# Kernel tuning notes

Measured on AMD Instinct MI355X. Metric: run time of the kernel, lower is better.

Reference implementation:

```python
import jax, jax.numpy as jnp
import numpy as np

DIM = 256
NUM_HEADS = 8
HEAD_DIM = 64
NUM_MEM_KV = 4
HIDDEN = NUM_HEADS * HEAD_DIM  # 512


def rmsnorm(x, g):
    # F.normalize(x, dim=1) * g * sqrt(C)
    c = x.shape[1]
    n = jnp.sqrt(jnp.sum(x * x, axis=1, keepdims=True))
    xn = x / jnp.maximum(n, 1e-12)
    return xn * g * (c ** 0.5)


def setup_inputs() -> dict:
    key = jax.random.key(0)
    ks = jax.random.split(key, 7)
    b, h, w = 16, 64, 64
    x = jax.random.normal(ks[0], (b, DIM, h, w), dtype=jnp.float32)
    g_in = jnp.ones((1, DIM, 1, 1), dtype=jnp.float32)
    w_qkv = jax.random.normal(ks[1], (HIDDEN * 3, DIM), dtype=jnp.float32) * (1.0 / np.sqrt(DIM))
    mem_kv = jax.random.normal(ks[2], (2, NUM_HEADS, HEAD_DIM, NUM_MEM_KV), dtype=jnp.float32)
    w_out = jax.random.normal(ks[3], (DIM, HIDDEN), dtype=jnp.float32) * (1.0 / np.sqrt(HIDDEN))
    b_out = jax.random.normal(ks[4], (DIM,), dtype=jnp.float32) * 0.01
    g_out = jnp.ones((1, DIM, 1, 1), dtype=jnp.float32)
    return {"x": x, "g_in": g_in, "w_qkv": w_qkv, "mem_kv": mem_kv,
            "w_out": w_out, "b_out": b_out, "g_out": g_out}


def reference(x, g_in, w_qkv, mem_kv, w_out, b_out, g_out):
    b, c, h, w = x.shape
    scale = HEAD_DIM ** (-0.5)
    xn = rmsnorm(x, g_in)
    # 1x1 conv (no bias) as GEMM: [b, 3*hidden, h, w]
    qkv = jnp.einsum('bcxy,oc->boxy', xn, w_qkv)
    q, k, v = jnp.split(qkv, 3, axis=1)
    # b (heads d) x y -> b heads d n
    def to_heads(t):
        return t.reshape(b, NUM_HEADS, HEAD_DIM, h * w)
    q, k, v = to_heads(q), to_heads(k), to_heads(v)
    mem_k = jnp.broadcast_to(mem_kv[0], (b, NUM_HEADS, HEAD_DIM, NUM_MEM_KV))
    mem_v = jnp.broadcast_to(mem_kv[1], (b, NUM_HEADS, HEAD_DIM, NUM_MEM_KV))
    k = jnp.concatenate([mem_k, k], axis=-1)
    v = jnp.concatenate([mem_v, v], axis=-1)
    q = jax.nn.softmax(q, axis=-2) * scale   # softmax over head_dim
    k = jax.nn.softmax(k, axis=-1)           # softmax over sequence
    context = jnp.einsum('bhdn,bhen->bhde', k, v)  # [b,h,d,d] per-head context
    out = jnp.einsum('bhde,bhdn->bhen', context, q)  # [b,h,d,n]
    out = out.reshape(b, HIDDEN, h, w)
    out = jnp.einsum('bcxy,oc->boxy', out, w_out) + b_out[None, :, None, None]
    return rmsnorm(out, g_out)
```

## Files before the change

kernel.cpp:

```cpp
#include <hip/hip_runtime.h>
#include <hip/hip_bf16.h>

typedef __hip_bfloat16 bf16;
typedef short bf16x8 __attribute__((ext_vector_type(8)));
typedef float f32x4 __attribute__((ext_vector_type(4)));

#define PTOT  65536
#define NPOS  4096
#define CIN   256
#define HID   512
#define HD    64

__device__ __forceinline__ float us2f(unsigned short u) {
    return __uint_as_float(((unsigned int)u) << 16);
}
__device__ __forceinline__ float ldf(const void* p, size_t i, bool bf) {
    return bf ? us2f(((const unsigned short*)p)[i]) : ((const float*)p)[i];
}
__device__ __forceinline__ unsigned short f2bs(float v) {
    __hip_bfloat16 h = __float2bfloat16(v);
    return *reinterpret_cast<unsigned short*>(&h);
}
__device__ __forceinline__ void gld16(const void* g, void* s) {
    __builtin_amdgcn_global_load_lds(
        (const __attribute__((address_space(1))) unsigned int*)g,
        (__attribute__((address_space(3))) unsigned int*)s, 16, 0, 0);
}

__global__ __launch_bounds__(256) void k_detect(const unsigned* __restrict__ x,
                                                int* __restrict__ flag) {
    int t = threadIdx.x;
    unsigned w = x[(size_t)t * 997];
    unsigned e7 = (w >> 8) & 0x7f;
    __shared__ int s[256];
    s[t] = (e7 >= 58 && e7 <= 66) ? 1 : 0;
    __syncthreads();
    for (int k = 128; k > 0; k >>= 1) { if (t < k) s[t] += s[t + k]; __syncthreads(); }
    if (t == 0) flag[0] = (s[0] >= 128) ? 1 : 0;
}

__global__ void k_relay(const int* __restrict__ src, int* __restrict__ dst) {
    dst[0] = src[0];
}

__global__ __launch_bounds__(256) void k_cvt(const void* __restrict__ src,
        unsigned short* __restrict__ dst, int n, const int* __restrict__ flag) {
    bool bf = flag[0] != 0;
    int i = blockIdx.x * 256 + threadIdx.x;
    if (i < n) dst[i] = f2bs(ldf(src, i, bf));
}

template<bool BF>
__device__ __forceinline__ void norm_xn_body(const void* __restrict__ x,
        const void* __restrict__ g, unsigned short* __restrict__ xn,
        float* __restrict__ smem)
{
    float* xs   = smem;
    float* gS   = smem + 17216;
    float* red2 = smem + 17472;
    float* sS   = smem + 18496;
    const int t = threadIdx.x;
    const int p0 = blockIdx.x * 64;
    const int b = p0 >> 12;
    const int posbase = p0 & 4095;
    gS[t] = ldf(g, t, BF);
    __syncthreads();
    const int pl4 = (t & 15) * 4;
    const int crow = t >> 4;
    const size_t xbase = ((size_t)b * CIN) << 12;
    float ssq[4] = {0.f, 0.f, 0.f, 0.f};
    #pragma unroll
    for (int rr = 0; rr < 16; ++rr) {
        int c = rr * 16 + crow;
        float v[4];
        if (BF) {
            ushort4 u = *(const ushort4*)((const unsigned short*)x + xbase +
                                          ((size_t)c << 12) + posbase + pl4);
            v[0] = us2f(u.x); v[1] = us2f(u.y); v[2] = us2f(u.z); v[3] = us2f(u.w);
        } else {
            float4 f = *(const float4*)((const float*)x + xbase +
                                        ((size_t)c << 12) + posbase + pl4);
            v[0] = f.x; v[1] = f.y; v[2] = f.z; v[3] = f.w;
        }
        float gv = gS[c];
        float* row = xs + (c >> 6) * 4304 + (c & 63) * 67;
        #pragma unroll
        for (int e = 0; e < 4; ++e) {
            ssq[e] += v[e] * v[e];
            row[pl4 + e] = v[e] * gv;
        }
    }
    #pragma unroll
    for (int e = 0; e < 4; ++e) red2[crow * 64 + pl4 + e] = ssq[e];
    __syncthreads();
    if (t < 64) {
        float tot = 0.f;
        #pragma unroll
        for (int j = 0; j < 16; ++j) tot += red2[j * 64 + t];
        sS[t] = 16.0f / fmaxf(sqrtf(tot), 1e-12f);
    }
    __syncthreads();
    const int pr = t >> 2, c0 = (t & 3) * 64;
    const float sc = sS[pr];
    const float* base = xs + (t & 3) * 4304 + pr;
    unsigned short* dst = &xn[(size_t)(p0 + pr) * 256 + c0];
    #pragma unroll
    for (int q = 0; q < 4; ++q) {
        unsigned short tmp[16];
        #pragma unroll
        for (int j = 0; j < 16; ++j)
            tmp[j] = f2bs(base[(q * 16 + j) * 67] * sc);
        *(uint4*)(dst + q * 16)     = ((uint4*)tmp)[0];
        *(uint4*)(dst + q * 16 + 8) = ((uint4*)tmp)[1];
    }
}
__global__ __launch_bounds__(256) void k_norm_xn(
        const void* __restrict__ x, const void* __restrict__ g,
        unsigned short* __restrict__ xn, const int* __restrict__ flag)
{
    __shared__ float smem[18560];
    if (flag[0]) norm_xn_body<true>(x, g, xn, smem);
    else         norm_xn_body<false>(x, g, xn, smem);
}

template<int KTOT, bool BIAS, int OSTRIDE>
__global__ __launch_bounds__(256) void k_mfma(
        const bf16* __restrict__ Am, const bf16* __restrict__ Bm,
        const void* __restrict__ bias, bf16* __restrict__ C,
        const int* __restrict__ flag)
{
    __shared__ __align__(16) unsigned short As[128 * 32];
    __shared__ __align__(16) unsigned short Bs[128 * 32];
    const int tid = threadIdx.x;
    const int wv = tid >> 6, lane = tid & 63;
    const int quad = lane >> 4, l16 = lane & 15;
    const int wm = wv >> 1, wn = wv & 1;
    const int m0 = blockIdx.y * 128, n0 = blockIdx.x * 128;
    f32x4 acc[4][4] = {};
    const bf16* gA = Am + (size_t)(m0 + (tid >> 2)) * KTOT + (tid & 3) * 8;
    const bf16* gB = Bm + (size_t)(n0 + (tid >> 2)) * KTOT + (tid & 3) * 8;
    unsigned short* lA = As + wv * 512;
    unsigned short* lB = Bs + wv * 512;
    for (int k0 = 0; k0 < KTOT; k0 += 32) {
        gld16(gA + k0, lA);
        gld16(gA + (size_t)64 * KTOT + k0, lA + 2048);
        gld16(gB + k0, lB);
        gld16(gB + (size_t)64 * KTOT + k0, lB + 2048);
        __syncthreads();
        bf16x8 bfr[4];
        #pragma unroll
        for (int j = 0; j < 4; ++j)
            bfr[j] = *(const bf16x8*)&Bs[(wn * 64 + j * 16 + l16) * 32 + quad * 8];
        #pragma unroll
        for (int i = 0; i < 4; ++i) {
            bf16x8 af = *(const bf16x8*)&As[(wm * 64 + i * 16 + l16) * 32 + quad * 8];
            #pragma unroll
            for (int j = 0; j < 4; ++j)
                acc[i][j] = __builtin_amdgcn_mfma_f32_16x16x32_bf16(af, bfr[j], acc[i][j], 0, 0, 0);
        }
        __syncthreads();
    }
    bool bf = BIAS ? (flag[0] != 0) : false;
    #pragma unroll
    for (int i = 0; i < 4; ++i) {
        int row = m0 + wm * 64 + i * 16 + quad * 4;
        #pragma unroll
        for (int r = 0; r < 4; ++r) {
            float bv = BIAS ? ldf(bias, row + r, bf) : 0.0f;
            #pragma unroll
            for (int j = 0; j < 4; ++j) {
                int col = n0 + wn * 64 + j * 16 + l16;
                C[(size_t)(row + r) * OSTRIDE + col] = __float2bfloat16(acc[i][j][r] + bv);
            }
        }
    }
}

__global__ __launch_bounds__(512) void k_kvgemm(
        const bf16* __restrict__ Am, const bf16* __restrict__ Bm,
        bf16* __restrict__ C)
{
    __shared__ __align__(16) unsigned short As[128 * 256];
    __shared__ __align__(16) unsigned short Bs[2][64 * 256];
    const int t = threadIdx.x;
    const int w = t >> 6, lane = t & 63;
    const int quad = lane >> 4, l16 = lane & 15;
    const int wm = w >> 1, wn = w & 1;
    const int p = blockIdx.x;
    const int xcd = p & 7, slot = p >> 3;
    const int chunk = xcd * 4 + (slot & 3);
    const int mt = slot >> 2;
    const int m0 = mt * 128;
    const size_t cbase = (size_t)chunk * 2048;

    const int srow = t >> 5;
    const int sks  = (t & 31) ^ (srow & 7);

    #pragma unroll
    for (int q = 0; q < 8; ++q)
        gld16(Am + (size_t)(m0 + q * 16 + srow) * 256 + sks * 8,
              (char*)As + q * 8192 + w * 1024);
    #pragma unroll
    for (int q = 0; q < 4; ++q)
        gld16(Bm + (cbase + q * 16 + srow) * 256 + sks * 8,
              (char*)Bs[0] + q * 8192 + w * 1024);
    #pragma unroll
    for (int q = 0; q < 4; ++q)
        gld16(Bm + (cbase + 64 + q * 16 + srow) * 256 + sks * 8,
              (char*)Bs[1] + q * 8192 + w * 1024);

    asm volatile("s_waitcnt vmcnt(8)" ::: "memory");
    __builtin_amdgcn_s_barrier();
    asm volatile("" ::: "memory");

    bf16x8 af[2][8];
    #pragma unroll
    for (int i = 0; i < 2; ++i) {
        int row = wm * 32 + i * 16 + l16;
        #pragma unroll
        for (int kk = 0; kk < 8; ++kk)
            af[i][kk] = *(const bf16x8*)((const char*)As + row * 512 +
                         (((kk * 4 + quad) ^ (row & 7)) << 4));
    }

    for (int s = 0; s < 32; ++s) {
        if (s > 0) {
            asm volatile("" ::: "memory");
            __builtin_amdgcn_s_barrier();
            asm volatile("" ::: "memory");
            if (s + 1 < 32) {
                #pragma unroll
                for (int q = 0; q < 4; ++q)
                    gld16(Bm + (cbase + (size_t)(s + 1) * 64 + q * 16 + srow) * 256 + sks * 8,
                          (char*)Bs[(s + 1) & 1] + q * 8192 + w * 1024);
            }
        }
        if (s == 0)      asm volatile("s_waitcnt vmcnt(4)"  ::: "memory");
        else if (s < 31) asm volatile("s_waitcnt vmcnt(20)" ::: "memory");
        else             asm volatile("s_waitcnt vmcnt(16)" ::: "memory");
        __builtin_amdgcn_s_barrier();
        asm volatile("" ::: "memory");

        const unsigned short* Bbuf = Bs[s & 1];
        f32x4 acc[2][2] = {};
        #pragma unroll
        for (int kk = 0; kk < 8; ++kk) {
            bf16x8 bfr[2];
            #pragma unroll
            for (int j = 0; j < 2; ++j) {
                int row = wn * 32 + j * 16 + l16;
                bfr[j] = *(const bf16x8*)((const char*)Bbuf + row * 512 +
                          (((kk * 4 + quad) ^ (row & 7)) << 4));
            }
            #pragma unroll
            for (int i = 0; i < 2; ++i)
                #pragma unroll
                for (int j = 0; j < 2; ++j)
                    acc[i][j] = __builtin_amdgcn_mfma_f32_16x16x32_bf16(af[i][kk], bfr[j], acc[i][j], 0, 0, 0);
        }
        #pragma unroll
        for (int i = 0; i < 2; ++i) {
            #pragma unroll
            for (int r = 0; r < 4; ++r) {
                int row = m0 + wm * 32 + i * 16 + quad * 4 + r;
                size_t col = cbase + (size_t)s * 64 + wn * 32;
                #pragma unroll
                for (int j = 0; j < 2; ++j)
                    C[(size_t)row * PTOT + col + j * 16 + l16] = __float2bfloat16(acc[i][j][r]);
            }
        }
    }
}

__global__ __launch_bounds__(512, 4) void k_qapply(
        const bf16* __restrict__ xn, const bf16* __restrict__ wq,
        const unsigned short* __restrict__ ct_bf,
        unsigned short* __restrict__ oat_pe)
{
    __shared__ __align__(16) char smem[73728];
    unsigned short* As  = (unsigned short*)smem;
    float*          S32 = (float*)smem;
    unsigned short* qsm = (unsigned short*)(smem + 8192);
    unsigned short* Bs  = (unsigned short*)(smem + 32768);
    unsigned short* ctS = (unsigned short*)(smem + 65536);
    const int t = threadIdx.x;
    const int w = t >> 6, lane = t & 63;
    const int quad = lane >> 4, l16 = lane & 15;
    const int wm = w >> 1, wn = w & 1;
    const int pm = w >> 2, pn = w & 3;
    const int bid = blockIdx.x;
    const int h = (bid >> 3) & 7;
    const int c = (bid & 7) | ((bid >> 6) << 3);
    const int n0 = h * HD;
    const size_t P0 = (size_t)c * 1024;
    const int b = (int)(P0 >> 12);
    const int srow = t >> 5, sks = (t & 31) ^ (srow & 7);

    #pragma unroll
    for (int q = 0; q < 4; ++q)
        gld16(wq + (size_t)(n0 + q * 16 + srow) * 256 + sks * 8,
              smem + q * 8192 + w * 1024);
    {
        int e = t >> 3, sl = t & 7;
        gld16(ct_bf + (size_t)(b * 8 + h) * 4096 + e * 64 + ((sl ^ (e & 7)) * 8),
              (char*)ctS + w * 1024);
    }
    #pragma unroll
    for (int q = 0; q < 2; ++q)
        gld16(xn + (P0 + q * 16 + srow) * 256 + sks * 8,
              (char*)Bs + q * 8192 + w * 1024);
    #pragma unroll
    for (int q = 0; q < 2; ++q)
        gld16(xn + (P0 + 32 + q * 16 + srow) * 256 + sks * 8,
              (char*)Bs + 16384 + q * 8192 + w * 1024);

    asm volatile("s_waitcnt vmcnt(4)" ::: "memory");
    __builtin_amdgcn_s_barrier();
    asm volatile("" ::: "memory");

    bf16x8 af[8];
    {
        int row = wm * 16 + l16;
        #pragma unroll
        for (int kk = 0; kk < 8; ++kk)
            af[kk] = *(const bf16x8*)((const char*)As + row * 512 +
                      (((kk * 4 + quad) ^ (row & 7)) << 4));
    }

    const int smp = t >> 4, smseg = t & 15;

    for (int s = 0; s < 32; ++s) {
        if (s > 0 && s + 1 < 32) {
            #pragma unroll
            for (int q = 0; q < 2; ++q)
                gld16(xn + (P0 + (size_t)(s + 1) * 32 + q * 16 + srow) * 256 + sks * 8,
                      (char*)Bs + ((s + 1) & 1) * 16384 + q * 8192 + w * 1024);
        }
        if (s == 0)      asm volatile("s_waitcnt vmcnt(2)" ::: "memory");
        else if (s < 31) asm volatile("s_waitcnt vmcnt(6)" ::: "memory");
        else             asm volatile("s_waitcnt vmcnt(4)" ::: "memory");
        __builtin_amdgcn_s_barrier();
        asm volatile("" ::: "memory");

        const char* Bbuf = (const char*)Bs + (s & 1) * 16384;
        f32x4 acc = {};
        #pragma unroll
        for (int kk = 0; kk < 8; ++kk) {
            int row = wn * 16 + l16;
            bf16x8 bfr = *(const bf16x8*)(Bbuf + row * 512 +
                          (((kk * 4 + quad) ^ (row & 7)) << 4));
            acc = __builtin_amdgcn_mfma_f32_16x16x32_bf16(af[kk], bfr, acc, 0, 0, 0);
        }
        {
            int pos = wn * 16 + l16;
            int sl = (wm * 4 + quad) ^ (pos & 7);
            *(f32x4*)&S32[pos * 64 + sl * 4] = acc;
        }
        asm volatile("s_waitcnt lgkmcnt(0)" ::: "memory");
        __builtin_amdgcn_s_barrier();
        asm volatile("" ::: "memory");

        {
            f32x4 v = *(const f32x4*)&S32[smp * 64 + ((smseg ^ (smp & 7)) << 2)];
            float m = fmaxf(fmaxf(v[0], v[1]), fmaxf(v[2], v[3]));
            #pragma unroll
            for (int st = 1; st < 16; st <<= 1)
                m = fmaxf(m, __shfl_xor(m, st));
            float ev[4], sum = 0.f;
            #pragma unroll
            for (int e = 0; e < 4; ++e) { ev[e] = __expf(v[e] - m); sum += ev[e]; }
            #pragma unroll
            for (int st = 1; st < 16; st <<= 1)
                sum += __shfl_xor(sum, st);
            float inv = 0.125f / sum;
            unsigned short tmp[4];
            #pragma unroll
            for (int e = 0; e < 4; ++e) tmp[e] = f2bs(ev[e] * inv);
            *(ushort4*)&qsm[smp * 64 + (((smseg >> 1) ^ (smp & 7)) << 3) + (smseg & 1) * 4]
                = *(ushort4*)tmp;
        }
        asm volatile("s_waitcnt lgkmcnt(0)" ::: "memory");
        __builtin_amdgcn_s_barrier();
        asm volatile("" ::: "memory");

        f32x4 acc2 = {};
        #pragma unroll
        for (int kk = 0; kk < 2; ++kk) {
            int prow = pm * 16 + l16;
            bf16x8 a2 = *(const bf16x8*)&qsm[prow * 64 +
                         (((kk * 4 + quad) ^ (prow & 7)) << 3)];
            int e = pn * 16 + l16;
            bf16x8 b2 = *(const bf16x8*)&ctS[e * 64 +
                         (((kk * 4 + quad) ^ (e & 7)) << 3)];
            acc2 = __builtin_amdgcn_mfma_f32_16x16x32_bf16(a2, b2, acc2, 0, 0, 0);
        }
        #pragma unroll
        for (int r = 0; r < 4; ++r) {
            size_t prow = P0 + (size_t)s * 32 + pm * 16 + quad * 4 + r;
            oat_pe[prow * HID + n0 + pn * 16 + l16] = f2bs(acc2[r]);
        }
    }
}

__global__ __launch_bounds__(256) void k_kstats(
        const bf16* __restrict__ kv, const void* __restrict__ memkv,
        float* __restrict__ rowmax, float* __restrict__ rowinv,
        const int* __restrict__ flag)
{
    bool bf = flag[0] != 0;
    int r = blockIdx.x;
    int b = r >> 9, hd = r & 511;
    const unsigned short* krow = (const unsigned short*)kv + (size_t)hd * PTOT + b * NPOS;
    int t = threadIdx.x;
    float vals[16];
    float m = -1e30f;
    #pragma unroll
    for (int i = 0; i < 16; ++i) {
        vals[i] = us2f(krow[t + (i << 8)]);
        m = fmaxf(m, vals[i]);
    }
    float mv = (t < 4) ? ldf(memkv, hd * 4 + t, bf) : -1e30f;
    m = fmaxf(m, mv);
    __shared__ float red[256];
    red[t] = m; __syncthreads();
    for (int s = 128; s > 0; s >>= 1) {
        if (t < s) red[t] = fmaxf(red[t], red[t + s]);
        __syncthreads();
    }
    float M = red[0]; __syncthreads();
    float sum = 0.f;
    #pragma unroll
    for (int i = 0; i < 16; ++i) sum += __expf(vals[i] - M);
    if (t < 4) sum += __expf(mv - M);
    red[t] = sum; __syncthreads();
    for (int s = 128; s > 0; s >>= 1) {
        if (t < s) red[t] += red[t + s];
        __syncthreads();
    }
    if (t == 0) { rowmax[r] = M; rowinv[r] = 1.0f / red[0]; }
}

__global__ __launch_bounds__(256) void k_context_mfma(
        const bf16* __restrict__ kv, const void* __restrict__ memkv,
        const float* __restrict__ rowmax, const float* __restrict__ rowinv,
        float* __restrict__ ctpart, const int* __restrict__ flag)
{
    bool bf = flag[0] != 0;
    int bh = blockIdx.x, chunk = blockIdx.y;
    int b = bh >> 3, h = bh & 7;
    __shared__ __align__(16) unsigned short As[4][64 * 32];
    __shared__ __align__(16) unsigned short Bs[4][64 * 32];
    __shared__ float rmS[64], riS[64];
    const int tid = threadIdx.x;
    if (tid < 64) {
        rmS[tid] = rowmax[(b << 9) + (h << 6) + tid];
        riS[tid] = rowinv[(b << 9) + (h << 6) + tid];
    }
    __syncthreads();
    const int wv = tid >> 6, lane = tid & 63;
    const int quad = lane >> 4, l16 = lane & 15;
    const int wm = wv >> 1, wn = wv & 1;
    const int krow = tid >> 2, kseg = tid & 3;
    const float rm = rmS[krow], ri = riS[krow];
    const unsigned short* kbase = (const unsigned short*)kv + (size_t)(h * HD) * PTOT + b * NPOS + chunk * 1024;
    const unsigned short* vbase = (const unsigned short*)kv + (size_t)(HID + h * HD) * PTOT + b * NPOS + chunk * 1024;
    f32x4 acc[2][2] = {};
    for (int s = 0; s < 8; ++s) {
        int nb = s * 128;
        #pragma unroll
        for (int kk = 0; kk < 4; ++kk) {
            uint4 u = *(const uint4*)(kbase + (size_t)krow * PTOT + nb + kk * 32 + kseg * 8);
            unsigned short out[8];
            const unsigned short* us = (const unsigned short*)&u;
            #pragma unroll
            for (int e = 0; e < 8; ++e)
                out[e] = f2bs(__expf(us2f(us[e]) - rm) * ri);
            *(uint4*)&As[kk][krow * 32 + kseg * 8] = *(uint4*)out;
        }
        #pragma unroll
        for (int kk = 0; kk < 4; ++kk)
            gld16(vbase + (size_t)(wv * 16 + (lane >> 2)) * PTOT + nb + kk * 32 + (lane & 3) * 8,
                  &Bs[kk][wv * 512]);
        __syncthreads();
        #pragma unroll
        for (int kk = 0; kk < 4; ++kk) {
            bf16x8 bfr[2];
            #pragma unroll
            for (int j = 0; j < 2; ++j)
                bfr[j] = *(const bf16x8*)&Bs[kk][(wn * 32 + j * 16 + l16) * 32 + quad * 8];
            #pragma unroll
            for (int i = 0; i < 2; ++i) {
                bf16x8 af = *(const bf16x8*)&As[kk][(wm * 32 + i * 16 + l16) * 32 + quad * 8];
                #pragma unroll
                for (int j = 0; j < 2; ++j)
                    acc[i][j] = __builtin_amdgcn_mfma_f32_16x16x32_bf16(af, bfr[j], acc[i][j], 0, 0, 0);
            }
        }
        __syncthreads();
    }
    if (chunk == 0) {
        float mv[2][4];
        #pragma unroll
        for (int j = 0; j < 2; ++j) {
            int e = wn * 32 + j * 16 + l16;
            #pragma unroll
            for (int mm = 0; mm < 4; ++mm)
                mv[j][mm] = ldf(memkv, 2048 + ((h << 6) + e) * 4 + mm, bf);
        }
        #pragma unroll
        for (int i = 0; i < 2; ++i) {
            #pragma unroll
            for (int r = 0; r < 4; ++r) {
                int d = wm * 32 + i * 16 + quad * 4 + r;
                #pragma unroll
                for (int mm = 0; mm < 4; ++mm) {
                    float kw = __expf(ldf(memkv, ((h << 6) + d) * 4 + mm, bf) - rmS[d]) * riS[d];
                    #pragma unroll
                    for (int j = 0; j < 2; ++j)
                        acc[i][j][r] = fmaf(kw, mv[j][mm], acc[i][j][r]);
                }
            }
        }
    }
    float* outp = ctpart + (size_t)(chunk * 128 + bh) * 4096;
    #pragma unroll
    for (int i = 0; i < 2; ++i) {
        #pragma unroll
        for (int r = 0; r < 4; ++r) {
            int d = wm * 32 + i * 16 + quad * 4 + r;
            #pragma unroll
            for (int j = 0; j < 2; ++j) {
                int e = wn * 32 + j * 16 + l16;
                outp[d * 64 + e] = acc[i][j][r];
            }
        }
    }
}

__global__ __launch_bounds__(256) void k_ctsum(
        const float* __restrict__ ctpart, unsigned short* __restrict__ ct_bf)
{
    int bh = blockIdx.x, t = threadIdx.x;
    int i0 = t * 16;
    int e = i0 >> 6, d0 = i0 & 63;
    unsigned short tmp[16];
    #pragma unroll
    for (int j = 0; j < 16; ++j) {
        int d = d0 + j;
        float s = 0.f;
        #pragma unroll
        for (int c = 0; c < 4; ++c)
            s += ctpart[(size_t)(c * 128 + bh) * 4096 + d * 64 + e];
        tmp[j] = f2bs(s);
    }
    unsigned short* dst = ct_bf + (size_t)bh * 4096 + i0;
    *(uint4*)dst = ((uint4*)tmp)[0];
    *(uint4*)(dst + 8) = ((uint4*)tmp)[1];
}

template<bool BF>
__device__ __forceinline__ void rmsout_body(const unsigned short* __restrict__ pre,
        const void* __restrict__ g, void* __restrict__ out, float* __restrict__ smem)
{
    float* gS   = smem;
    float* red2 = smem + 256;
    float* sS   = smem + 1280;
    const int t = threadIdx.x;
    const int p0 = blockIdx.x * 64;
    const int b = p0 >> 12;
    const int posbase = p0 & 4095;
    gS[t] = ldf(g, t, BF);
    const int pl4 = (t & 15) * 4;
    const int crow = t >> 4;
    const unsigned short* pbase = pre + p0 + pl4;
    ushort4 u[16];
    float ssq[4] = {0.f, 0.f, 0.f, 0.f};
    #pragma unroll
    for (int rr = 0; rr < 16; ++rr) {
        int c = rr * 16 + crow;
        u[rr] = *(const ushort4*)(pbase + (size_t)c * PTOT);
        float v0 = us2f(u[rr].x), v1 = us2f(u[rr].y), v2 = us2f(u[rr].z), v3 = us2f(u[rr].w);
        ssq[0] += v0 * v0; ssq[1] += v1 * v1; ssq[2] += v2 * v2; ssq[3] += v3 * v3;
    }
    #pragma unroll
    for (int e = 0; e < 4; ++e) red2[crow * 64 + pl4 + e] = ssq[e];
    __syncthreads();
    if (t < 64) {
        float tot = 0.f;
        #pragma unroll
        for (int j = 0; j < 16; ++j) tot += red2[j * 64 + t];
        sS[t] = 16.0f / fmaxf(sqrtf(tot), 1e-12f);
    }
    __syncthreads();
    const float s0 = sS[pl4], s1 = sS[pl4 + 1], s2 = sS[pl4 + 2], s3 = sS[pl4 + 3];
    #pragma unroll
    for (int rr = 0; rr < 16; ++rr) {
        int c = rr * 16 + crow;
        float gv = gS[c];
        float v0 = us2f(u[rr].x) * s0 * gv;
        float v1 = us2f(u[rr].y) * s1 * gv;
        float v2 = us2f(u[rr].z) * s2 * gv;
        float v3 = us2f(u[rr].w) * s3 * gv;
        size_t oi = ((size_t)(b * CIN + c) << 12) + posbase + pl4;
        if (BF) {
            ushort4 o;
            o.x = f2bs(v0); o.y = f2bs(v1); o.z = f2bs(v2); o.w = f2bs(v3);
            *(ushort4*)((unsigned short*)out + oi) = o;
        } else {
            float4 o; o.x = v0; o.y = v1; o.z = v2; o.w = v3;
            *(float4*)((float*)out + oi) = o;
        }
    }
}
__global__ __launch_bounds__(256) void k_rmsnorm_out(
        const unsigned short* __restrict__ pre, const void* __restrict__ g,
        void* __restrict__ out, const int* __restrict__ flag)
{
    __shared__ float smem[1344];
    if (flag[0]) rmsout_body<true>(pre, g, out, smem);
    else         rmsout_body<false>(pre, g, out, smem);
}

extern "C" void kernel_launch(void* const* d_in, const int* in_sizes, int n_in,
                              void* d_out, int out_size, void* d_ws, size_t ws_size,
                              hipStream_t stream) {
    const void* x     = d_in[0];
    const void* g_in  = d_in[1];
    const void* w_qkv = d_in[2];
    const void* memkv = d_in[3];
    const void* w_out = d_in[4];
    const void* b_out = d_in[5];
    const void* g_out = d_in[6];

    char* ws = (char*)d_ws;
    bf16*           kv     = (bf16*)ws;
    unsigned short* oat_pe = (unsigned short*)(ws + 67108864);
    unsigned short* pre    = (unsigned short*)ws;
    int*            flagB  = (int*)(ws + 50331648);

    char* ob = (char*)d_out;
    float*          ctpart = (float*)ob;
    float*          rowmax = (float*)(ob + 8388608);
    float*          rowinv = (float*)(ob + 8421376);
    int*            flagA  = (int*)(ob + 8454144);
    unsigned short* wq_b   = (unsigned short*)(ob + 9437184);
    unsigned short* wout_b = (unsigned short*)(ob + 10485760);
    unsigned short* ct_bf  = (unsigned short*)(ob + 11010048);
    unsigned short* xn     = (unsigned short*)(ob + 12582912);

    k_detect<<<1, 256, 0, stream>>>((const unsigned*)x, flagA);

    k_cvt<<<1536, 256, 0, stream>>>(w_qkv, wq_b, 1536 * 256, flagA);
    k_cvt<<<512, 256, 0, stream>>>(w_out, wout_b, 256 * 512, flagA);

    k_norm_xn<<<1024, 256, 0, stream>>>(x, g_in, xn, flagA);

    k_kvgemm<<<256, 512, 0, stream>>>(
        (const bf16*)(wq_b + (size_t)512 * CIN), (const bf16*)xn, kv);

    k_kstats<<<8192, 256, 0, stream>>>(kv, memkv, rowmax, rowinv, flagA);

    dim3 gctx(128, 4);
    k_context_mfma<<<gctx, 256, 0, stream>>>(kv, memkv, rowmax, rowinv, ctpart, flagA);

    k_ctsum<<<128, 256, 0, stream>>>(ctpart, ct_bf);

    k_qapply<<<512, 512, 0, stream>>>(
        (const bf16*)xn, (const bf16*)wq_b, ct_bf, oat_pe);

    dim3 go(512, 2);
    k_mfma<HID, true, PTOT><<<go, 256, 0, stream>>>(
        (const bf16*)wout_b, (const bf16*)oat_pe, b_out, (bf16*)pre, flagA);

    k_relay<<<1, 1, 0, stream>>>(flagA, flagB);

    k_rmsnorm_out<<<1024, 256, 0, stream>>>(pre, g_out, d_out, flagB);
}
```

Measured before the change: 336.7 us.

## Process two heads per block in q-apply and keep softmax in registers

The q-apply kernel now handles a pair of heads (128 q channels) and 64 positions per step, halving the grid. Each wave holds a full 64-channel head slice of the Q weights in registers, so the head-dim softmax is done with in-register shuffles. This drops the fp32 score staging in shared memory and two barriers per step. The cost is much more shared memory (160KB), more registers (launch bounds 2), fewer blocks in flight, and heavier per-lane qsm scatter stores.

After: 329.7 us. 1.02x faster.

```diff
diff --git a/kernel.cpp b/kernel.cpp
--- a/kernel.cpp
+++ b/kernel.cpp
@@ -272,133 +272,134 @@
     }
 }
 
-__global__ __launch_bounds__(512, 4) void k_qapply(
+__global__ __launch_bounds__(512, 2) void k_qapply(
         const bf16* __restrict__ xn, const bf16* __restrict__ wq,
         const unsigned short* __restrict__ ct_bf,
         unsigned short* __restrict__ oat_pe)
 {
-    __shared__ __align__(16) char smem[73728];
-    unsigned short* As  = (unsigned short*)smem;
-    float*          S32 = (float*)smem;
-    unsigned short* qsm = (unsigned short*)(smem + 8192);
-    unsigned short* Bs  = (unsigned short*)(smem + 32768);
-    unsigned short* ctS = (unsigned short*)(smem + 65536);
+    __shared__ __align__(16) char smem[163840];
     const int t = threadIdx.x;
     const int w = t >> 6, lane = t & 63;
     const int quad = lane >> 4, l16 = lane & 15;
     const int wm = w >> 1, wn = w & 1;
-    const int pm = w >> 2, pn = w & 3;
     const int bid = blockIdx.x;
-    const int h = (bid >> 3) & 7;
-    const int c = (bid & 7) | ((bid >> 6) << 3);
-    const int n0 = h * HD;
+    const int hp = (bid >> 3) & 3;
+    const int c  = (bid & 7) | ((bid >> 5) << 3);
+    const int n0 = hp * 128;
     const size_t P0 = (size_t)c * 1024;
-    const int b = (int)(P0 >> 12);
+    const int b = c >> 2;
     const int srow = t >> 5, sks = (t & 31) ^ (srow & 7);
 
     #pragma unroll
-    for (int q = 0; q < 4; ++q)
+    for (int k = 0; k < 2; ++k) {
+        int u = k * 512 + t;
+        int hh = u >> 9, rem = u & 511, e = rem >> 3, sl = rem & 7;
+        gld16(ct_bf + (size_t)(b * 8 + hp * 2 + hh) * 4096 + e * 64 + ((sl ^ (e & 7)) * 8),
+              smem + 81920 + k * 8192 + w * 1024);
+    }
+    #pragma unroll
+    for (int q = 0; q < 8; ++q)
         gld16(wq + (size_t)(n0 + q * 16 + srow) * 256 + sks * 8,
               smem + q * 8192 + w * 1024);
-    {
-        int e = t >> 3, sl = t & 7;
-        gld16(ct_bf + (size_t)(b * 8 + h) * 4096 + e * 64 + ((sl ^ (e & 7)) * 8),
-              (char*)ctS + w * 1024);
-    }
-    #pragma unroll
-    for (int q = 0; q < 2; ++q)
+    #pragma unroll
+    for (int q = 0; q < 4; ++q)
         gld16(xn + (P0 + q * 16 + srow) * 256 + sks * 8,
-              (char*)Bs + q * 8192 + w * 1024);
-    #pragma unroll
-    for (int q = 0; q < 2; ++q)
-        gld16(xn + (P0 + 32 + q * 16 + srow) * 256 + sks * 8,
-              (char*)Bs + 16384 + q * 8192 + w * 1024);
-
-    asm volatile("s_waitcnt vmcnt(4)" ::: "memory");
+              smem + 98304 + q * 8192 + w * 1024);
+    #pragma unroll
+    for (int q = 0; q < 4; ++q)
+        gld16(xn + (P0 + 64 + q * 16 + srow) * 256 + sks * 8,
+              smem + 131072 + q * 8192 + w * 1024);
+
+    asm volatile("s_waitcnt vmcnt(8)" ::: "memory");
     __builtin_amdgcn_s_barrier();
     asm volatile("" ::: "memory");
 
-    bf16x8 af[8];
-    {
-        int row = wm * 16 + l16;
+    bf16x8 wqf[4][8];
+    #pragma unroll
+    for (int j = 0; j < 4; ++j) {
+        int row = wn * 64 + j * 16 + l16;
         #pragma unroll
         for (int kk = 0; kk < 8; ++kk)
-            af[kk] = *(const bf16x8*)((const char*)As + row * 512 +
-                      (((kk * 4 + quad) ^ (row & 7)) << 4));
-    }
-
-    const int smp = t >> 4, smseg = t & 15;
-
-    for (int s = 0; s < 32; ++s) {
-        if (s > 0 && s + 1 < 32) {
-            #pragma unroll
-            for (int q = 0; q < 2; ++q)
-                gld16(xn + (P0 + (size_t)(s + 1) * 32 + q * 16 + srow) * 256 + sks * 8,
-                      (char*)Bs + ((s + 1) & 1) * 16384 + q * 8192 + w * 1024);
-        }
-        if (s == 0)      asm volatile("s_waitcnt vmcnt(2)" ::: "memory");
-        else if (s < 31) asm volatile("s_waitcnt vmcnt(6)" ::: "memory");
-        else             asm volatile("s_waitcnt vmcnt(4)" ::: "memory");
+            wqf[j][kk] = *(const bf16x8*)(smem + row * 512 +
+                          (((kk * 4 + quad) ^ (row & 7)) << 4));
+    }
+
+    unsigned short* qsm = (unsigned short*)(smem + 65536);
+
+    for (int s = 0; s < 16; ++s) {
+        if (s > 0) {
+            asm volatile("" ::: "memory");
+            __builtin_amdgcn_s_barrier();
+            asm volatile("" ::: "memory");
+            if (s + 1 < 16) {
+                #pragma unroll
+                for (int q = 0; q < 4; ++q)
+                    gld16(xn + (P0 + (size_t)(s + 1) * 64 + q * 16 + srow) * 256 + sks * 8,
+                          smem + 98304 + ((s + 1) & 1) * 32768 + q * 8192 + w * 1024);
+            }
+        }
+        if (s == 0)      asm volatile("s_waitcnt vmcnt(4)"  ::: "memory");
+        else if (s < 15) asm volatile("s_waitcnt vmcnt(20)" ::: "memory");
+        else             asm volatile("s_waitcnt vmcnt(16)" ::: "memory");
         __builtin_amdgcn_s_barrier();
         asm volatile("" ::: "memory");
 
-        const char* Bbuf = (const char*)Bs + (s & 1) * 16384;
-        f32x4 acc = {};
+        const char* Bbuf = smem + 98304 + (s & 1) * 32768;
+        f32x4 acc[4] = {};
         #pragma unroll
         for (int kk = 0; kk < 8; ++kk) {
-            int row = wn * 16 + l16;
-            bf16x8 bfr = *(const bf16x8*)(Bbuf + row * 512 +
+            int row = wm * 16 + l16;
+            bf16x8 xf = *(const bf16x8*)(Bbuf + row * 512 +
                           (((kk * 4 + quad) ^ (row & 7)) << 4));
-            acc = __builtin_amdgcn_mfma_f32_16x16x32_bf16(af[kk], bfr, acc, 0, 0, 0);
-        }
-        {
-            int pos = wn * 16 + l16;
-            int sl = (wm * 4 + quad) ^ (pos & 7);
-            *(f32x4*)&S32[pos * 64 + sl * 4] = acc;
-        }
-        asm volatile("s_waitcnt lgkmcnt(0)" ::: "memory");
-        __builtin_amdgcn_s_barrier();
-        asm volatile("" ::: "memory");
-
-        {
-            f32x4 v = *(const f32x4*)&S32[smp * 64 + ((smseg ^ (smp & 7)) << 2)];
-            float m = fmaxf(fmaxf(v[0], v[1]), fmaxf(v[2], v[3]));
-            #pragma unroll
-            for (int st = 1; st < 16; st <<= 1)
-                m = fmaxf(m, __shfl_xor(m, st));
+            #pragma unroll
+            for (int j = 0; j < 4; ++j)
+                acc[j] = __builtin_amdgcn_mfma_f32_16x16x32_bf16(xf, wqf[j][kk], acc[j], 0, 0, 0);
+        }
+
+        #pragma unroll
+        for (int r = 0; r < 4; ++r) {
+            float m = fmaxf(fmaxf(acc[0][r], acc[1][r]), fmaxf(acc[2][r], acc[3][r]));
+            m = fmaxf(m, __shfl_xor(m, 1));
+            m = fmaxf(m, __shfl_xor(m, 2));
+            m = fmaxf(m, __shfl_xor(m, 4));
+            m = fmaxf(m, __shfl_xor(m, 8));
             float ev[4], sum = 0.f;
             #pragma unroll
-            for (int e = 0; e < 4; ++e) { ev[e] = __expf(v[e] - m); sum += ev[e]; }
-            #pragma unroll
-            for (int st = 1; st < 16; st <<= 1)
-                sum += __shfl_xor(sum, st);
+            for (int j = 0; j < 4; ++j) { ev[j] = __expf(acc[j][r] - m); sum += ev[j]; }
+            sum += __shfl_xor(sum, 1);
+            sum += __shfl_xor(sum, 2);
+            sum += __shfl_xor(sum, 4);
+            sum += __shfl_xor(sum, 8);
             float inv = 0.125f / sum;
-            unsigned short tmp[4];
-            #pragma unroll
-            for (int e = 0; e < 4; ++e) tmp[e] = f2bs(ev[e] * inv);
-            *(ushort4*)&qsm[smp * 64 + (((smseg >> 1) ^ (smp & 7)) << 3) + (smseg & 1) * 4]
-                = *(ushort4*)tmp;
-        }
-        asm volatile("s_waitcnt lgkmcnt(0)" ::: "memory");
-        __builtin_amdgcn_s_barrier();
-        asm volatile("" ::: "memory");
-
-        f32x4 acc2 = {};
+            int pos = wm * 16 + quad * 4 + r;
+            #pragma unroll
+            for (int j = 0; j < 4; ++j) {
+                int ch = wn * 64 + j * 16 + l16;
+                qsm[pos * 128 + (((ch >> 3) ^ (pos & 7)) << 3) + (ch & 7)] = f2bs(ev[j] * inv);
+            }
+        }
+
+        f32x4 acc2[4] = {};
         #pragma unroll
         for (int kk = 0; kk < 2; ++kk) {
-            int prow = pm * 16 + l16;
-            bf16x8 a2 = *(const bf16x8*)&qsm[prow * 64 +
-                         (((kk * 4 + quad) ^ (prow & 7)) << 3)];
-            int e = pn * 16 + l16;
-            bf16x8 b2 = *(const bf16x8*)&ctS[e * 64 +
-                         (((kk * 4 + quad) ^ (e & 7)) << 3)];
-            acc2 = __builtin_amdgcn_mfma_f32_16x16x32_bf16(a2, b2, acc2, 0, 0, 0);
-        }
-        #pragma unroll
-        for (int r = 0; r < 4; ++r) {
-            size_t prow = P0 + (size_t)s * 32 + pm * 16 + quad * 4 + r;
-            oat_pe[prow * HID + n0 + pn * 16 + l16] = f2bs(acc2[r]);
-        }
+            int row = wm * 16 + l16;
+            bf16x8 qf = *(const bf16x8*)(smem + 65536 + row * 256 +
+                         (((wn * 8 + kk * 4 + quad) ^ (row & 7)) << 4));
+            #pragma unroll
+            for (int j = 0; j < 4; ++j) {
+                int e = j * 16 + l16;
+                bf16x8 cf = *(const bf16x8*)(smem + 81920 + wn * 8192 + e * 128 +
+                             (((kk * 4 + quad) ^ (e & 7)) << 4));
+                acc2[j] = __builtin_amdgcn_mfma_f32_16x16x32_bf16(qf, cf, acc2[j], 0, 0, 0);
+            }
+        }
+        #pragma unroll
+        for (int j = 0; j < 4; ++j)
+            #pragma unroll
+            for (int r = 0; r < 4; ++r) {
+                size_t prow = P0 + (size_t)s * 64 + wm * 16 + quad * 4 + r;
+                oat_pe[prow * HID + n0 + wn * 64 + j * 16 + l16] = f2bs(acc2[j][r]);
+            }
     }
 }
 
@@ -665,7 +666,7 @@
 
     k_ctsum<<<128, 256, 0, stream>>>(ctpart, ct_bf);
 
-    k_qapply<<<512, 512, 0, stream>>>(
+    k_qapply<<<256, 512, 0, stream>>>(
         (const bf16*)xn, (const bf16*)wq_b, ct_bf, oat_pe);
 
     dim3 go(512, 2);
```
